# Kernel optimization log

Measured on AMD Instinct MI355X. Metric: run time of the kernel, lower is better.

The kernel has to match this reference:

```python
import jax, jax.numpy as jnp
import numpy as np

K = 8          # number of nearest neighbors (init kwarg k)
EPS = 1e-16    # torch_geometric clamps squared distance at 1e-16


def setup_inputs() -> dict:
    key = jax.random.key(0)
    k1, k2, k3, k4 = jax.random.split(key, 4)
    N, D, B = 16384, 128, 64
    x1 = jax.random.normal(k1, (N, 3 + D), dtype=jnp.float32)  # true graph: [coords(3) | feats(D)]
    x2 = jax.random.normal(k2, (N, 3 + D), dtype=jnp.float32)  # pred graph
    b1 = jnp.sort(jax.random.randint(k3, (N,), 0, B))          # sorted per-node graph ids
    b2 = jnp.sort(jax.random.randint(k4, (N,), 0, B))
    return {"x1": x1, "x2": x2, "b1": b1, "b2": b2}


def _knn_interpolate(f1, c1, c2, b1, b2, k):
    # Squared pairwise distances [N2, N1] via ||a||^2 + ||b||^2 - 2ab (GEMM form).
    d2 = (jnp.sum(c2 * c2, axis=-1)[:, None]
          + jnp.sum(c1 * c1, axis=-1)[None, :]
          - 2.0 * (c2 @ c1.T))
    d2 = jnp.maximum(d2, 0.0)
    # Batch-aware kNN: forbid cross-graph neighbors.
    d2 = jnp.where(b2[:, None] != b1[None, :], jnp.inf, d2)
    neg_d2, idx = jax.lax.top_k(-d2, k)          # k smallest distances per target node
    w = 1.0 / jnp.clip(-neg_d2, EPS)             # [N2, k] inverse-squared-distance weights
    nbr = f1[idx]                                # [N2, k, D] gather of neighbor features
    return jnp.einsum('nk,nkd->nd', w, nbr) / jnp.sum(w, axis=-1, keepdims=True)


def reference(x1, x2, b1, b2):
    c1, f1 = x1[:, :3], x1[:, 3:]
    c2, f2 = x2[:, :3], x2[:, 3:]
    f1_interp = _knn_interpolate(f1, c1, c2, b1, b2, K)
    return jnp.mean((f1_interp - f2) ** 2)
```

## Files before the change

kernel.cpp:

```cpp
#include <hip/hip_runtime.h>
#include <math.h>

#define KNN 8
#define QPB 16
#define SUB 16
#define BLK 256
#define CAP 1024
#define NBT 258

__launch_bounds__(BLK, 4)
__global__ void knn_fused(const float* __restrict__ x1,
                          const float* __restrict__ x2,
                          const int* __restrict__ b1,
                          const int* __restrict__ b2,
                          int N, int ROW,
                          float* __restrict__ ws_part) {
  __shared__ float4 c4[CAP];
  __shared__ int sstart[NBT];
  __shared__ int send[NBT];
  __shared__ int s_range[2];
  __shared__ float wred[BLK / 64];

  const int tid  = threadIdx.x;
  const int lane = tid & 63;
  const int wv   = tid >> 6;
  const int qi   = tid >> 4;
  const int sub  = tid & (SUB - 1);
  const int q0   = blockIdx.x * QPB;
  const int q    = q0 + qi;
  const int qlast = min(q0 + QPB - 1, N - 1);

  if (wv < 2) {
    const int target = (wv == 0) ? b2[q0] : (b2[qlast] + 1);
    int lo = 0, hi = N;
    while (lo < hi) {
      int step = (hi - lo + 63) >> 6;
      int p = lo + lane * step;
      bool pred = (p < hi) && (b1[p] < target);
      int c = __popcll(__ballot(pred));
      if (c == 0) { hi = lo; break; }
      int nlo = lo + (c - 1) * step + 1;
      hi = min(hi, lo + c * step);
      lo = nlo;
    }
    if (lane == 0) s_range[wv] = lo;
  }

  float qx = 0.f, qy = 0.f, qz = 0.f; int mybatch = -1;
  if (q < N) {
    const float* c2 = x2 + (size_t)q * ROW;
    qx = c2[0]; qy = c2[1]; qz = c2[2];
    mybatch = b2[q];
  }
  const float n2 = qx * qx + qy * qy + qz * qz;

  float dist[KNN]; int nidx[KNN];
#pragma unroll
  for (int k = 0; k < KNN; ++k) { dist[k] = INFINITY; nidx[k] = 0; }

  __syncthreads();
  const int s1 = s_range[0], e1 = s_range[1];

  for (int t0 = s1; t0 < e1; t0 += CAP) {
    const int t1 = min(t0 + CAP, e1);
    const int L  = t1 - t0;
    for (int i = tid; i < NBT; i += BLK) { sstart[i] = CAP; send[i] = 0; }
    __syncthreads();
    for (int i = t0 + tid; i < t1; i += BLK) {
      const float* p = x1 + (size_t)i * ROW;
      float cx = p[0], cy = p[1], cz = p[2];
      int li = i - t0;
      c4[li] = make_float4(cx, cy, cz, cx * cx + cy * cy + cz * cz);
      int bc = b1[i];
      int bp = (li == 0)     ? (bc ^ 1) : b1[i - 1];
      int bn = (li == L - 1) ? (bc ^ 1) : b1[i + 1];
      if (bc != bp) sstart[bc] = li;
      if (bc != bn) send[bc]  = li + 1;
    }
    __syncthreads();

    int lo = CAP, hi = 0;
    if (mybatch >= 0) { lo = sstart[mybatch]; hi = send[mybatch]; }
    int j = lo + sub;
    if (j < hi) {
      float4 c = c4[j];
      while (true) {
        int jn = j + SUB;
        bool more = jn < hi;
        float4 cn = c4[more ? jn : j];
        float d = fmaf(-2.0f, fmaf(qx, c.x, fmaf(qy, c.y, qz * c.z)), n2 + c.w);
        d = fmaxf(d, 0.0f);
        if (d < dist[KNN - 1]) {
          dist[KNN - 1] = d; nidx[KNN - 1] = t0 + j;
#pragma unroll
          for (int k = KNN - 1; k > 0; --k) {
            if (dist[k] < dist[k - 1]) {
              float td = dist[k]; dist[k] = dist[k - 1]; dist[k - 1] = td;
              int ti = nidx[k]; nidx[k] = nidx[k - 1]; nidx[k - 1] = ti;
            }
          }
        }
        if (!more) break;
        j = jn; c = cn;
      }
    }
  }

  float md[KNN]; int mi[KNN];
#pragma unroll
  for (int r = 0; r < KNN; ++r) {
    float hd = dist[0]; int hidx = nidx[0];
    float bd = hd; int bi = hidx;
#pragma unroll
    for (int m = 1; m <= 8; m <<= 1) {
      float od = __shfl_xor(bd, m); int oi = __shfl_xor(bi, m);
      if (od < bd || (od == bd && oi < bi)) { bd = od; bi = oi; }
    }
    md[r] = bd; mi[r] = bi;
    if (hd == bd && hidx == bi) {
#pragma unroll
      for (int k = 0; k < KNN - 1; ++k) { dist[k] = dist[k + 1]; nidx[k] = nidx[k + 1]; }
      dist[KNN - 1] = INFINITY; nidx[KNN - 1] = 0;
    }
  }

  float pacc = 0.0f;
#pragma unroll
  for (int qq = 0; qq < 4; ++qq) {
    int gq = q0 + wv * 4 + qq;
    if (gq < N) {
      float w[KNN]; int id[KNN]; float sw = 0.0f;
#pragma unroll
      for (int r = 0; r < KNN; ++r) {
        float dd = __shfl(md[r], qq * 16);
        id[r] = __shfl(mi[r], qq * 16);
        w[r] = 1.0f / fmaxf(dd, 1e-16f);
        sw += w[r];
      }
      float acc0 = 0.0f, acc1 = 0.0f;
#pragma unroll
      for (int r = 0; r < KNN; ++r) {
        const float* f = x1 + (size_t)id[r] * ROW + 3;
        acc0 += w[r] * f[lane];
        acc1 += w[r] * f[lane + 64];
      }
      const float* f2 = x2 + (size_t)gq * ROW + 3;
      float rinv = 1.0f / sw;
      float e0 = acc0 * rinv - f2[lane];
      float e1 = acc1 * rinv - f2[lane + 64];
      pacc += e0 * e0 + e1 * e1;
    }
  }
#pragma unroll
  for (int off = 32; off > 0; off >>= 1) pacc += __shfl_xor(pacc, off);
  if (lane == 0) wred[wv] = pacc;
  __syncthreads();
  if (tid == 0) {
    float s = (wred[0] + wred[1]) + (wred[2] + wred[3]);
    ws_part[blockIdx.x] = s;
  }
}

__global__ void knn_final(const float* __restrict__ part, int n,
                          float scale, float* __restrict__ out) {
  __shared__ float sm[256];
  float s = 0.0f;
  for (int i = threadIdx.x; i < n; i += 256) s += part[i];
  sm[threadIdx.x] = s;
  __syncthreads();
  for (int step = 128; step > 0; step >>= 1) {
    if (threadIdx.x < step) sm[threadIdx.x] += sm[threadIdx.x + step];
    __syncthreads();
  }
  if (threadIdx.x == 0) out[0] = sm[0] * scale;
}

extern "C" void kernel_launch(void* const* d_in, const int* in_sizes, int n_in,
                              void* d_out, int out_size, void* d_ws, size_t ws_size,
                              hipStream_t stream) {
  const float* x1 = (const float*)d_in[0];
  const float* x2 = (const float*)d_in[1];
  const int* b1 = (const int*)d_in[2];
  const int* b2 = (const int*)d_in[3];
  int N = in_sizes[2];
  int ROW = in_sizes[0] / N;
  float* out = (float*)d_out;

  int blocks = (N + QPB - 1) / QPB;
  float* ws_part = (float*)d_ws;
  if (ws_size < (size_t)blocks * sizeof(float)) return;

  knn_fused<<<blocks, BLK, 0, stream>>>(x1, x2, b1, b2, N, ROW, ws_part);
  float scale = 1.0f / ((float)N * (float)(ROW - 3));
  knn_final<<<1, 256, 0, stream>>>(ws_part, blocks, scale, out);
}
```

Before: 27.96 us.

## Use 32 lanes per query, binary-search batch ranges, fuse gather into merge

Halves queries per block to 8 and assigns 32 lanes per query, so each query's candidate scan is split across more threads. The per-tile shared-memory batch start/end tables are replaced by per-thread binary searches over b1, skipped when the whole block lies in one graph. The feature gather and weighted accumulation now happen inside the top-k merge loop, with each lane covering four strided feature columns, and the x2 features are prefetched early. Launch bounds now request higher occupancy, which may limit registers and cause spills.

```diff
diff --git a/kernel.cpp b/kernel.cpp
--- a/kernel.cpp
+++ b/kernel.cpp
@@ -2,13 +2,18 @@
 #include <math.h>
 
 #define KNN 8
-#define QPB 16
-#define SUB 16
+#define QPB 8
+#define SUB 32
 #define BLK 256
 #define CAP 1024
-#define NBT 258
 
-__launch_bounds__(BLK, 4)
+__device__ __forceinline__ int lbound_g(const int* __restrict__ a, int n, int v) {
+  int lo = 0, hi = n;
+  while (lo < hi) { int m = (lo + hi) >> 1; if (a[m] < v) lo = m + 1; else hi = m; }
+  return lo;
+}
+
+__launch_bounds__(BLK, 8)
 __global__ void knn_fused(const float* __restrict__ x1,
                           const float* __restrict__ x2,
                           const int* __restrict__ b1,
@@ -16,22 +21,22 @@
                           int N, int ROW,
                           float* __restrict__ ws_part) {
   __shared__ float4 c4[CAP];
-  __shared__ int sstart[NBT];
-  __shared__ int send[NBT];
-  __shared__ int s_range[2];
+  __shared__ int   s_info[4];
   __shared__ float wred[BLK / 64];
 
   const int tid  = threadIdx.x;
   const int lane = tid & 63;
   const int wv   = tid >> 6;
-  const int qi   = tid >> 4;
+  const int qi   = tid >> 5;
   const int sub  = tid & (SUB - 1);
+  const int dl   = lane & 31;
   const int q0   = blockIdx.x * QPB;
   const int q    = q0 + qi;
   const int qlast = min(q0 + QPB - 1, N - 1);
 
   if (wv < 2) {
-    const int target = (wv == 0) ? b2[q0] : (b2[qlast] + 1);
+    const int bb = (wv == 0) ? b2[q0] : b2[qlast];
+    const int target = bb + wv;
     int lo = 0, hi = N;
     while (lo < hi) {
       int step = (hi - lo + 63) >> 6;
@@ -43,14 +48,17 @@
       hi = min(hi, lo + c * step);
       lo = nlo;
     }
-    if (lane == 0) s_range[wv] = lo;
+    if (lane == 0) { s_info[wv] = lo; s_info[2 + wv] = bb; }
   }
 
   float qx = 0.f, qy = 0.f, qz = 0.f; int mybatch = -1;
+  float f2v0 = 0.f, f2v1 = 0.f, f2v2 = 0.f, f2v3 = 0.f;
   if (q < N) {
     const float* c2 = x2 + (size_t)q * ROW;
     qx = c2[0]; qy = c2[1]; qz = c2[2];
     mybatch = b2[q];
+    const float* f2 = c2 + 3 + dl;
+    f2v0 = f2[0]; f2v1 = f2[32]; f2v2 = f2[64]; f2v3 = f2[96];
   }
   const float n2 = qx * qx + qy * qy + qz * qz;
 
@@ -59,97 +67,75 @@
   for (int k = 0; k < KNN; ++k) { dist[k] = INFINITY; nidx[k] = 0; }
 
   __syncthreads();
-  const int s1 = s_range[0], e1 = s_range[1];
+  const int s1 = s_info[0], e1 = s_info[1];
+  const bool single = (s_info[2] == s_info[3]);
+
+  int qs = s1, qe = e1;
+  if (!single && q < N) {
+    qs = lbound_g(b1, N, mybatch);
+    qe = lbound_g(b1, N, mybatch + 1);
+  }
+  if (q >= N) { qs = 0; qe = 0; }
 
   for (int t0 = s1; t0 < e1; t0 += CAP) {
     const int t1 = min(t0 + CAP, e1);
-    const int L  = t1 - t0;
-    for (int i = tid; i < NBT; i += BLK) { sstart[i] = CAP; send[i] = 0; }
     __syncthreads();
     for (int i = t0 + tid; i < t1; i += BLK) {
       const float* p = x1 + (size_t)i * ROW;
       float cx = p[0], cy = p[1], cz = p[2];
-      int li = i - t0;
-      c4[li] = make_float4(cx, cy, cz, cx * cx + cy * cy + cz * cz);
-      int bc = b1[i];
-      int bp = (li == 0)     ? (bc ^ 1) : b1[i - 1];
-      int bn = (li == L - 1) ? (bc ^ 1) : b1[i + 1];
-      if (bc != bp) sstart[bc] = li;
-      if (bc != bn) send[bc]  = li + 1;
+      c4[i - t0] = make_float4(cx, cy, cz, cx * cx + cy * cy + cz * cz);
     }
     __syncthreads();
-
-    int lo = CAP, hi = 0;
-    if (mybatch >= 0) { lo = sstart[mybatch]; hi = send[mybatch]; }
-    int j = lo + sub;
-    if (j < hi) {
-      float4 c = c4[j];
-      while (true) {
-        int jn = j + SUB;
-        bool more = jn < hi;
-        float4 cn = c4[more ? jn : j];
-        float d = fmaf(-2.0f, fmaf(qx, c.x, fmaf(qy, c.y, qz * c.z)), n2 + c.w);
-        d = fmaxf(d, 0.0f);
-        if (d < dist[KNN - 1]) {
-          dist[KNN - 1] = d; nidx[KNN - 1] = t0 + j;
+    const int lo = max(qs, t0), hi = min(qe, t1);
+    for (int j = lo + sub; j < hi; j += SUB) {
+      float4 c = c4[j - t0];
+      float d = fmaf(-2.0f, fmaf(qx, c.x, fmaf(qy, c.y, qz * c.z)), n2 + c.w);
+      d = fmaxf(d, 0.0f);
+      if (d < dist[KNN - 1]) {
+        dist[KNN - 1] = d; nidx[KNN - 1] = j;
 #pragma unroll
-          for (int k = KNN - 1; k > 0; --k) {
-            if (dist[k] < dist[k - 1]) {
-              float td = dist[k]; dist[k] = dist[k - 1]; dist[k - 1] = td;
-              int ti = nidx[k]; nidx[k] = nidx[k - 1]; nidx[k - 1] = ti;
-            }
+        for (int k = KNN - 1; k > 0; --k) {
+          if (dist[k] < dist[k - 1]) {
+            float td = dist[k]; dist[k] = dist[k - 1]; dist[k - 1] = td;
+            int ti = nidx[k]; nidx[k] = nidx[k - 1]; nidx[k - 1] = ti;
           }
         }
-        if (!more) break;
-        j = jn; c = cn;
       }
     }
   }
 
-  float md[KNN]; int mi[KNN];
+  float acc0 = 0.f, acc1 = 0.f, acc2 = 0.f, acc3 = 0.f, sw = 0.f;
 #pragma unroll
   for (int r = 0; r < KNN; ++r) {
     float hd = dist[0]; int hidx = nidx[0];
     float bd = hd; int bi = hidx;
 #pragma unroll
-    for (int m = 1; m <= 8; m <<= 1) {
+    for (int m = 1; m <= 16; m <<= 1) {
       float od = __shfl_xor(bd, m); int oi = __shfl_xor(bi, m);
       if (od < bd || (od == bd && oi < bi)) { bd = od; bi = oi; }
     }
-    md[r] = bd; mi[r] = bi;
     if (hd == bd && hidx == bi) {
 #pragma unroll
       for (int k = 0; k < KNN - 1; ++k) { dist[k] = dist[k + 1]; nidx[k] = nidx[k + 1]; }
       dist[KNN - 1] = INFINITY; nidx[KNN - 1] = 0;
     }
+    float w = 1.0f / fmaxf(bd, 1e-16f);
+    sw += w;
+    const float* f = x1 + (size_t)bi * ROW + 3 + dl;
+    acc0 += w * f[0];
+    acc1 += w * f[32];
+    acc2 += w * f[64];
+    acc3 += w * f[96];
   }
 
   float pacc = 0.0f;
-#pragma unroll
-  for (int qq = 0; qq < 4; ++qq) {
-    int gq = q0 + wv * 4 + qq;
-    if (gq < N) {
-      float w[KNN]; int id[KNN]; float sw = 0.0f;
-#pragma unroll
-      for (int r = 0; r < KNN; ++r) {
-        float dd = __shfl(md[r], qq * 16);
-        id[r] = __shfl(mi[r], qq * 16);
-        w[r] = 1.0f / fmaxf(dd, 1e-16f);
-        sw += w[r];
-      }
-      float acc0 = 0.0f, acc1 = 0.0f;
-#pragma unroll
-      for (int r = 0; r < KNN; ++r) {
-        const float* f = x1 + (size_t)id[r] * ROW + 3;
-        acc0 += w[r] * f[lane];
-        acc1 += w[r] * f[lane + 64];
-      }
-      const float* f2 = x2 + (size_t)gq * ROW + 3;
-      float rinv = 1.0f / sw;
-      float e0 = acc0 * rinv - f2[lane];
-      float e1 = acc1 * rinv - f2[lane + 64];
-      pacc += e0 * e0 + e1 * e1;
-    }
+  if (q < N) {
+    float rinv = 1.0f / sw;
+    float e0 = acc0 * rinv - f2v0;
+    float e1 = acc1 * rinv - f2v1;
+    float e2 = acc2 * rinv - f2v2;
+    float e3 = acc3 * rinv - f2v3;
+    pacc = (e0 * e0 + e1 * e1) + (e2 * e2 + e3 * e3);
   }
 #pragma unroll
   for (int off = 32; off > 0; off >>= 1) pacc += __shfl_xor(pacc, off);
```

New measurement: 33.26 us. 1.19x slower.
